# Kernel optimization log

Measured on AMD Instinct MI355X. Metric: run time of the kernel, lower is better.

Reference implementation:

```python
import jax, jax.numpy as jnp
import numpy as np

N, IN_DIM, OUT_DIM = 100000, 256, 256
EPS = 1e-6

def setup_inputs() -> dict:
    key = jax.random.key(0)
    ks = jax.random.split(key, 7)
    s = 1.0 / np.sqrt(IN_DIM)
    x = jax.random.normal(ks[0], (N, IN_DIM), dtype=jnp.float32)
    Wq = jax.random.uniform(ks[1], (IN_DIM, OUT_DIM), jnp.float32, -s, s)
    bq = jax.random.uniform(ks[2], (OUT_DIM,), jnp.float32, -s, s)
    Wk = jax.random.uniform(ks[3], (IN_DIM, OUT_DIM), jnp.float32, -s, s)
    bk = jax.random.uniform(ks[4], (OUT_DIM,), jnp.float32, -s, s)
    Wv = jax.random.uniform(ks[5], (IN_DIM, OUT_DIM), jnp.float32, -s, s)
    bv = jax.random.uniform(ks[6], (OUT_DIM,), jnp.float32, -s, s)
    return {"x": x, "Wq": Wq, "bq": bq, "Wk": Wk, "bk": bk, "Wv": Wv, "bv": bv}

def reference(x, Wq, bq, Wk, bk, Wv, bv):
    Q = jax.nn.relu(x @ Wq + bq)          # [N, d]
    K = jax.nn.relu(x @ Wk + bk)          # [N, d]
    V = x @ Wv + bv                       # [N, d]
    KV = jnp.einsum('nd,ne->de', K, V)    # [d, d]
    out = Q @ KV                          # [N, d]
    normalizer = Q @ K.sum(axis=0)[:, None].reshape(-1) [..., None] if False else (Q @ K.sum(axis=0)[:, None]) + EPS  # [N, 1]
    return out / normalizer
```

## Files before the change

### kernel.cpp

```cpp
#include <hip/hip_runtime.h>

typedef unsigned short u16;
typedef float f32x4 __attribute__((ext_vector_type(4)));
typedef short s16x8 __attribute__((ext_vector_type(8)));
typedef unsigned short u16x4 __attribute__((ext_vector_type(4)));

#define EPS 1e-6f

static __device__ __forceinline__ u16 f2bf(float f) {
  unsigned u = __float_as_uint(f);
  u += 0x7fffu + ((u >> 16) & 1u);
  return (u16)(u >> 16);
}
static __device__ __forceinline__ float bf2f(u16 h) {
  return __uint_as_float(((unsigned)h) << 16);
}

__global__ void wtrans_kernel(const float* __restrict__ Wq, const float* __restrict__ Wk,
                              const float* __restrict__ Wv,
                              u16* __restrict__ WqT, u16* __restrict__ WkT, u16* __restrict__ WvT) {
  int b = blockIdx.x;
  int mat = b >> 4, cg = b & 15;
  const float* W = mat == 0 ? Wq : (mat == 1 ? Wk : Wv);
  u16* WT = mat == 0 ? WqT : (mat == 1 ? WkT : WvT);
  int t = threadIdx.x;
  int c = cg * 16 + (t & 15);
  int k0 = (t >> 4) * 16;
  for (int i = 0; i < 16; ++i) {
    int k = k0 + i;
    WT[c * 256 + k] = f2bf(W[k * 256 + c]);
  }
}

__global__ __launch_bounds__(256, 2)
void qkv_kernel(const float* __restrict__ x,
                const u16* __restrict__ WqT, const u16* __restrict__ WkT, const u16* __restrict__ WvT,
                const float* __restrict__ bq, const float* __restrict__ bk, const float* __restrict__ bv,
                u16* __restrict__ Qb, u16* __restrict__ Kt, u16* __restrict__ Vt,
                float* __restrict__ ksum, int N, int NPAD) {
  __shared__ u16 xs[128][264];
  __shared__ u16 wst[128][40];
  __shared__ float ksl[256];
  const int tid = threadIdx.x;
  const int n0 = blockIdx.x * 128;

  ksl[tid] = 0.f;

  for (int i = 0; i < 32; ++i) {
    int l = tid + i * 256;
    int row = l >> 6;
    int c4 = (l & 63) << 2;
    int n = n0 + row;
    float4 v = make_float4(0.f, 0.f, 0.f, 0.f);
    if (n < N) v = *(const float4*)(x + (size_t)n * 256 + c4);
    u16x4 pk;
    pk[0] = f2bf(v.x); pk[1] = f2bf(v.y); pk[2] = f2bf(v.z); pk[3] = f2bf(v.w);
    *(u16x4*)&xs[row][c4] = pk;
  }

  const int wave = tid >> 6, lane = tid & 63;
  const int quad = lane >> 4, l16 = lane & 15;
  const int wr = (wave >> 1) * 64;
  const int wc = (wave & 1) * 64;

  const int scol = tid >> 1, sseg = (tid & 1) * 16;

  s16x8 w0, w1;
  {
    const u16* p = WqT + (size_t)scol * 256 + sseg;
    w0 = *(const s16x8*)p;
    w1 = *(const s16x8*)(p + 8);
  }

  f32x4 acc[4][4] = {};
  for (int it = 0; it < 48; ++it) {
    const int ph = it >> 3, kc = (it & 7) * 32;
    const int mat = ph >> 1;
    const int colBase = (ph & 1) * 128;

    __syncthreads();
    *(s16x8*)&wst[scol][sseg] = w0;
    *(s16x8*)&wst[scol][sseg + 8] = w1;
    __syncthreads();

    if (it + 1 < 48) {
      int itn = it + 1;
      int phn = itn >> 3, kcn = (itn & 7) * 32;
      int matn = phn >> 1, colBn = (phn & 1) * 128;
      const u16* WTn = matn == 0 ? WqT : (matn == 1 ? WkT : WvT);
      const u16* p = WTn + (size_t)(colBn + scol) * 256 + kcn + sseg;
      w0 = *(const s16x8*)p;
      w1 = *(const s16x8*)(p + 8);
    }

    s16x8 a[4], b[4];
    for (int f = 0; f < 4; ++f) a[f] = *(const s16x8*)&xs[wr + f * 16 + l16][kc + quad * 8];
    for (int f = 0; f < 4; ++f) b[f] = *(const s16x8*)&wst[wc + f * 16 + l16][quad * 8];
    for (int fr = 0; fr < 4; ++fr)
      for (int fc = 0; fc < 4; ++fc)
        acc[fr][fc] = __builtin_amdgcn_mfma_f32_16x16x32_bf16(a[fr], b[fc], acc[fr][fc], 0, 0, 0);

    if ((it & 7) == 7) {
      const float* bias = mat == 0 ? bq : (mat == 1 ? bk : bv);
      float ksacc[4] = {0.f, 0.f, 0.f, 0.f};
      for (int fc = 0; fc < 4; ++fc) {
        int colg = colBase + wc + fc * 16 + l16;
        float bb = bias[colg];
        for (int fr = 0; fr < 4; ++fr) {
          int nl = wr + fr * 16 + quad * 4;
          int n = n0 + nl;
          if (mat == 0) {
            for (int j = 0; j < 4; ++j) {
              float v = acc[fr][fc][j] + bb;
              v = fmaxf(v, 0.f);
              Qb[(size_t)(n + j) * 256 + colg] = (n + j < N) ? f2bf(v) : (u16)0;
            }
          } else {
            u16x4 pk;
            for (int j = 0; j < 4; ++j) {
              float v = acc[fr][fc][j] + bb;
              if (mat == 1) v = fmaxf(v, 0.f);
              bool ok = (n + j < N);
              pk[j] = ok ? f2bf(v) : (u16)0;
              if (mat == 1) ksacc[fc] += ok ? v : 0.f;
            }
            u16* T = (mat == 1) ? Kt : Vt;
            *(u16x4*)&T[(size_t)colg * NPAD + n] = pk;
          }
        }
      }
      if (mat == 1) {
        for (int fc = 0; fc < 4; ++fc) {
          float v = ksacc[fc];
          v += __shfl_xor(v, 16);
          v += __shfl_xor(v, 32);
          if (quad == 0) atomicAdd(&ksl[colBase + wc + fc * 16 + l16], v);
        }
      }
      for (int fr = 0; fr < 4; ++fr)
        for (int fc = 0; fc < 4; ++fc)
          acc[fr][fc] = (f32x4){0.f, 0.f, 0.f, 0.f};
    }
  }
  __syncthreads();
  atomicAdd(&ksum[tid], ksl[tid]);
}

__global__ __launch_bounds__(256, 2)
void kv_kernel(const u16* __restrict__ Kt, const u16* __restrict__ Vt,
               float* __restrict__ P, int NPAD) {
  __shared__ u16 As[128][40];
  __shared__ u16 Bs[128][40];
  const int tid = threadIdx.x;
  const int s = blockIdx.x & 63;
  const int tile = blockIdx.x >> 6;
  const int ti = (tile >> 1) * 128;
  const int tj = (tile & 1) * 128;
  const int wave = tid >> 6, lane = tid & 63;
  const int quad = lane >> 4, l16 = lane & 15;
  const int we = (wave >> 1) * 64;
  const int wd = (wave & 1) * 64;
  f32x4 acc[4][4] = {};
  const int NCH = NPAD >> 5;

  int row0 = (tid * 2) >> 2, seg0 = ((tid * 2) & 3) * 8;
  int row1 = (tid * 2 + 1) >> 2, seg1 = ((tid * 2 + 1) & 3) * 8;

  s16x8 ra0, ra1, rb0, rb1;
  int c = s;
  if (c < NCH) {
    int nb = c << 5;
    ra0 = *(const s16x8*)&Vt[(size_t)(ti + row0) * NPAD + nb + seg0];
    ra1 = *(const s16x8*)&Vt[(size_t)(ti + row1) * NPAD + nb + seg1];
    rb0 = *(const s16x8*)&Kt[(size_t)(tj + row0) * NPAD + nb + seg0];
    rb1 = *(const s16x8*)&Kt[(size_t)(tj + row1) * NPAD + nb + seg1];
  }
  for (; c < NCH; c += 64) {
    __syncthreads();
    *(s16x8*)&As[row0][seg0] = ra0;
    *(s16x8*)&As[row1][seg1] = ra1;
    *(s16x8*)&Bs[row0][seg0] = rb0;
    *(s16x8*)&Bs[row1][seg1] = rb1;
    __syncthreads();
    int cn = c + 64;
    if (cn < NCH) {
      int nb = cn << 5;
      ra0 = *(const s16x8*)&Vt[(size_t)(ti + row0) * NPAD + nb + seg0];
      ra1 = *(const s16x8*)&Vt[(size_t)(ti + row1) * NPAD + nb + seg1];
      rb0 = *(const s16x8*)&Kt[(size_t)(tj + row0) * NPAD + nb + seg0];
      rb1 = *(const s16x8*)&Kt[(size_t)(tj + row1) * NPAD + nb + seg1];
    }
    s16x8 a[4], b[4];
    for (int f = 0; f < 4; ++f) a[f] = *(const s16x8*)&As[we + f * 16 + l16][quad * 8];
    for (int f = 0; f < 4; ++f) b[f] = *(const s16x8*)&Bs[wd + f * 16 + l16][quad * 8];
    for (int fr = 0; fr < 4; ++fr)
      for (int fc = 0; fc < 4; ++fc)
        acc[fr][fc] = __builtin_amdgcn_mfma_f32_16x16x32_bf16(a[fr], b[fc], acc[fr][fc], 0, 0, 0);
  }
  float* Pp = P + (size_t)s * 65536;
  for (int fr = 0; fr < 4; ++fr)
    for (int fc = 0; fc < 4; ++fc) {
      int d = tj + wd + fc * 16 + l16;
      int e0 = ti + we + fr * 16 + quad * 4;
      *(f32x4*)&Pp[(size_t)d * 256 + e0] = acc[fr][fc];
    }
}

__global__ void kvred_kernel(const float* __restrict__ P, u16* __restrict__ KVtb) {
  int d = blockIdx.x;
  int e = threadIdx.x;
  float s = 0.f;
  for (int sp = 0; sp < 64; ++sp) s += P[(size_t)sp * 65536 + d * 256 + e];
  KVtb[e * 256 + d] = f2bf(s);
}

__global__ __launch_bounds__(256, 2)
void out_kernel(const u16* __restrict__ Qb, const u16* __restrict__ KVtb,
                const float* __restrict__ ksum, float* __restrict__ out,
                int N, int NPAD) {
  __shared__ u16 Qs[128][264];
  __shared__ u16 KVs[128][40];
  __shared__ float nrm[128];
  __shared__ float ks[256];
  __shared__ float nrmp[256];
  const int tid = threadIdx.x;
  const int r0 = blockIdx.x * 128;

  for (int i = 0; i < 16; ++i) {
    int l = tid + i * 256;
    int row = l >> 5;
    int seg = (l & 31) << 3;
    *(s16x8*)&Qs[row][seg] = *(const s16x8*)&Qb[(size_t)(r0 + row) * 256 + seg];
  }
  ks[tid] = ksum[tid];
  __syncthreads();

  {
    int r = tid & 127, h = tid >> 7;
    float sa = 0.f;
    for (int d = h * 128; d < h * 128 + 128; d += 8) {
      s16x8 q = *(const s16x8*)&Qs[r][d];
      for (int j = 0; j < 8; ++j) sa += bf2f((u16)q[j]) * ks[d + j];
    }
    nrmp[tid] = sa;
  }
  __syncthreads();
  if (tid < 128) nrm[tid] = nrmp[tid] + nrmp[tid + 128] + EPS;

  const int wave = tid >> 6, lane = tid & 63;
  const int quad = lane >> 4, l16 = lane & 15;
  const int we = (wave >> 1) * 64;
  const int wrw = (wave & 1) * 64;
  const int scol = tid >> 1, sseg = (tid & 1) * 16;

  s16x8 w0, w1;
  {
    const u16* p = KVtb + (size_t)scol * 256 + sseg;
    w0 = *(const s16x8*)p;
    w1 = *(const s16x8*)(p + 8);
  }

  f32x4 acc[4][4] = {};
  for (int it = 0; it < 16; ++it) {
    const int eh = it >> 3, kc = (it & 7) * 32;

    __syncthreads();
    *(s16x8*)&KVs[scol][sseg] = w0;
    *(s16x8*)&KVs[scol][sseg + 8] = w1;
    __syncthreads();

    if (it + 1 < 16) {
      int itn = it + 1;
      int ehn = itn >> 3, kcn = (itn & 7) * 32;
      const u16* p = KVtb + (size_t)(ehn * 128 + scol) * 256 + kcn + sseg;
      w0 = *(const s16x8*)p;
      w1 = *(const s16x8*)(p + 8);
    }

    s16x8 a[4], b[4];
    for (int f = 0; f < 4; ++f) a[f] = *(const s16x8*)&KVs[we + f * 16 + l16][quad * 8];
    for (int f = 0; f < 4; ++f) b[f] = *(const s16x8*)&Qs[wrw + f * 16 + l16][kc + quad * 8];
    for (int fr = 0; fr < 4; ++fr)
      for (int fc = 0; fc < 4; ++fc)
        acc[fr][fc] = __builtin_amdgcn_mfma_f32_16x16x32_bf16(a[fr], b[fc], acc[fr][fc], 0, 0, 0);

    if ((it & 7) == 7) {
      for (int fc = 0; fc < 4; ++fc) {
        int rl = wrw + fc * 16 + l16;
        int rg = r0 + rl;
        float inv = 1.0f / nrm[rl];
        if (rg < N) {
          for (int fr = 0; fr < 4; ++fr) {
            int eg = eh * 128 + we + fr * 16 + quad * 4;
            f32x4 o;
            o[0] = acc[fr][fc][0] * inv;
            o[1] = acc[fr][fc][1] * inv;
            o[2] = acc[fr][fc][2] * inv;
            o[3] = acc[fr][fc][3] * inv;
            *(f32x4*)&out[(size_t)rg * 256 + eg] = o;
          }
        }
      }
      for (int fr = 0; fr < 4; ++fr)
        for (int fc = 0; fc < 4; ++fc)
          acc[fr][fc] = (f32x4){0.f, 0.f, 0.f, 0.f};
    }
  }
}

extern "C" void kernel_launch(void* const* d_in, const int* in_sizes, int n_in,
                              void* d_out, int out_size, void* d_ws, size_t ws_size,
                              hipStream_t stream) {
  const float* x  = (const float*)d_in[0];
  const float* Wq = (const float*)d_in[1];
  const float* bq = (const float*)d_in[2];
  const float* Wk = (const float*)d_in[3];
  const float* bk = (const float*)d_in[4];
  const float* Wv = (const float*)d_in[5];
  const float* bv = (const float*)d_in[6];
  float* out = (float*)d_out;

  int N = in_sizes[0] / 256;
  int NPAD = ((N + 127) / 128) * 128;
  int nblk = NPAD / 128;

  char* p = (char*)d_ws;
  size_t szT = (size_t)256 * NPAD * sizeof(u16);
  u16* Kt = (u16*)p; p += szT;
  u16* Vt = (u16*)p; p += szT;
  u16* Qb = (u16*)p; p += szT;
  float* P = (float*)p; p += (size_t)64 * 65536 * sizeof(float);
  u16* KVtb = (u16*)p; p += (size_t)65536 * sizeof(u16);
  float* ksum = (float*)p; p += 256 * sizeof(float);
  u16* WqT = (u16*)p; p += (size_t)65536 * sizeof(u16);
  u16* WkT = (u16*)p; p += (size_t)65536 * sizeof(u16);
  u16* WvT = (u16*)p; p += (size_t)65536 * sizeof(u16);

  hipMemsetAsync(ksum, 0, 256 * sizeof(float), stream);
  wtrans_kernel<<<48, 256, 0, stream>>>(Wq, Wk, Wv, WqT, WkT, WvT);
  qkv_kernel<<<nblk, 256, 0, stream>>>(x, WqT, WkT, WvT, bq, bk, bv, Qb, Kt, Vt, ksum, N, NPAD);
  kv_kernel<<<256, 256, 0, stream>>>(Kt, Vt, P, NPAD);
  kvred_kernel<<<256, 256, 0, stream>>>(P, KVtb);
  out_kernel<<<nblk, 256, 0, stream>>>(Qb, KVtb, ksum, out, N, NPAD);
}
```

Before: 377.5 us.

## Double-buffer QKV and KV GEMM stages, enlarge QKV tiles, widen KV split

The QKV projection kernel now processes 256 rows per block with 512 threads and double-buffers the weight tile in shared memory, so each k-step needs one barrier instead of two. The Q epilogue uses swapped MFMA operands so Q can be stored as packed 4-element rows. The KV reduction kernel gets double-buffered shared tiles and a split factor of 128 when workspace allows, which doubles its grid. The trade-offs are higher LDS use per block, fewer QKV blocks in flight, and more partial sums for the reduce kernel to read.

Result: slower. 413.7 us (+9.6%).

```diff
diff --git a/kernel.cpp b/kernel.cpp
--- a/kernel.cpp
+++ b/kernel.cpp
@@ -32,22 +32,22 @@
   }
 }
 
-__global__ __launch_bounds__(256, 2)
+__global__ __launch_bounds__(512, 2)
 void qkv_kernel(const float* __restrict__ x,
                 const u16* __restrict__ WqT, const u16* __restrict__ WkT, const u16* __restrict__ WvT,
                 const float* __restrict__ bq, const float* __restrict__ bk, const float* __restrict__ bv,
                 u16* __restrict__ Qb, u16* __restrict__ Kt, u16* __restrict__ Vt,
                 float* __restrict__ ksum, int N, int NPAD) {
-  __shared__ u16 xs[128][264];
-  __shared__ u16 wst[128][40];
+  __shared__ u16 xs[256][264];
+  __shared__ u16 wst[2][128][40];
   __shared__ float ksl[256];
   const int tid = threadIdx.x;
-  const int n0 = blockIdx.x * 128;
-
-  ksl[tid] = 0.f;
+  const int n0 = blockIdx.x * 256;
+
+  if (tid < 256) ksl[tid] = 0.f;
 
   for (int i = 0; i < 32; ++i) {
-    int l = tid + i * 256;
+    int l = tid + i * 512;
     int row = l >> 6;
     int c4 = (l & 63) << 2;
     int n = n0 + row;
@@ -63,97 +63,125 @@
   const int wr = (wave >> 1) * 64;
   const int wc = (wave & 1) * 64;
 
-  const int scol = tid >> 1, sseg = (tid & 1) * 16;
-
-  s16x8 w0, w1;
-  {
-    const u16* p = WqT + (size_t)scol * 256 + sseg;
-    w0 = *(const s16x8*)p;
-    w1 = *(const s16x8*)(p + 8);
-  }
+  const int scol = tid >> 2, sseg = (tid & 3) * 8;
+
+  auto cptr = [&](int it) -> const u16* {
+    int ph = it >> 3, kc = (it & 7) * 32;
+    int mat = ph >> 1, colB = (ph & 1) * 128;
+    const u16* WT = mat == 0 ? WqT : (mat == 1 ? WkT : WvT);
+    return WT + (size_t)(colB + scol) * 256 + kc + sseg;
+  };
+
+#define QKV_MFMA(BUF, SWAP) { \
+    s16x8 a[4], b[4]; \
+    _Pragma("unroll") for (int f = 0; f < 4; ++f) a[f] = *(const s16x8*)&xs[wr + f * 16 + l16][kc + quad * 8]; \
+    _Pragma("unroll") for (int f = 0; f < 4; ++f) b[f] = *(const s16x8*)&wst[BUF][wc + f * 16 + l16][quad * 8]; \
+    if (SWAP) { \
+      _Pragma("unroll") for (int fr = 0; fr < 4; ++fr) \
+      _Pragma("unroll") for (int fc = 0; fc < 4; ++fc) \
+        acc[fr][fc] = __builtin_amdgcn_mfma_f32_16x16x32_bf16(b[fr], a[fc], acc[fr][fc], 0, 0, 0); \
+    } else { \
+      _Pragma("unroll") for (int fr = 0; fr < 4; ++fr) \
+      _Pragma("unroll") for (int fc = 0; fc < 4; ++fc) \
+        acc[fr][fc] = __builtin_amdgcn_mfma_f32_16x16x32_bf16(a[fr], b[fc], acc[fr][fc], 0, 0, 0); \
+    } }
+
+  s16x8 w0 = *(const s16x8*)cptr(0);
+  s16x8 w1 = *(const s16x8*)cptr(1);
+  *(s16x8*)&wst[0][scol][sseg] = w0;
 
   f32x4 acc[4][4] = {};
-  for (int it = 0; it < 48; ++it) {
-    const int ph = it >> 3, kc = (it & 7) * 32;
-    const int mat = ph >> 1;
-    const int colBase = (ph & 1) * 128;
-
-    __syncthreads();
-    *(s16x8*)&wst[scol][sseg] = w0;
-    *(s16x8*)&wst[scol][sseg + 8] = w1;
-    __syncthreads();
-
-    if (it + 1 < 48) {
-      int itn = it + 1;
-      int phn = itn >> 3, kcn = (itn & 7) * 32;
-      int matn = phn >> 1, colBn = (phn & 1) * 128;
-      const u16* WTn = matn == 0 ? WqT : (matn == 1 ? WkT : WvT);
-      const u16* p = WTn + (size_t)(colBn + scol) * 256 + kcn + sseg;
-      w0 = *(const s16x8*)p;
-      w1 = *(const s16x8*)(p + 8);
-    }
-
-    s16x8 a[4], b[4];
-    for (int f = 0; f < 4; ++f) a[f] = *(const s16x8*)&xs[wr + f * 16 + l16][kc + quad * 8];
-    for (int f = 0; f < 4; ++f) b[f] = *(const s16x8*)&wst[wc + f * 16 + l16][quad * 8];
-    for (int fr = 0; fr < 4; ++fr)
-      for (int fc = 0; fc < 4; ++fc)
-        acc[fr][fc] = __builtin_amdgcn_mfma_f32_16x16x32_bf16(a[fr], b[fc], acc[fr][fc], 0, 0, 0);
-
-    if ((it & 7) == 7) {
-      const float* bias = mat == 0 ? bq : (mat == 1 ? bk : bv);
-      float ksacc[4] = {0.f, 0.f, 0.f, 0.f};
-      for (int fc = 0; fc < 4; ++fc) {
-        int colg = colBase + wc + fc * 16 + l16;
-        float bb = bias[colg];
-        for (int fr = 0; fr < 4; ++fr) {
-          int nl = wr + fr * 16 + quad * 4;
-          int n = n0 + nl;
-          if (mat == 0) {
-            for (int j = 0; j < 4; ++j) {
-              float v = acc[fr][fc][j] + bb;
-              v = fmaxf(v, 0.f);
-              Qb[(size_t)(n + j) * 256 + colg] = (n + j < N) ? f2bf(v) : (u16)0;
+  for (int ii = 0; ii < 24; ++ii) {
+    {
+      const int it = 2 * ii;
+      const int kc = (it & 7) * 32;
+      const bool swapQ = (it < 16);
+      __syncthreads();
+      if (it < 46) w0 = *(const s16x8*)cptr(it + 2);
+      QKV_MFMA(0, swapQ);
+      *(s16x8*)&wst[1][scol][sseg] = w1;
+    }
+    {
+      const int it = 2 * ii + 1;
+      const int kc = (it & 7) * 32;
+      const int ph = it >> 3;
+      const int mat = ph >> 1, colBase = (ph & 1) * 128;
+      __syncthreads();
+      if (it < 46) w1 = *(const s16x8*)cptr(it + 2);
+      QKV_MFMA(1, (mat == 0));
+      if (it < 47) *(s16x8*)&wst[0][scol][sseg] = w0;
+
+      if ((it & 7) == 7) {
+        const float* bias = mat == 0 ? bq : (mat == 1 ? bk : bv);
+        if (mat == 0) {
+#pragma unroll
+          for (int fw = 0; fw < 4; ++fw) {
+            int colg4 = colBase + wc + fw * 16 + quad * 4;
+            float4 bb = *(const float4*)(bias + colg4);
+#pragma unroll
+            for (int fx = 0; fx < 4; ++fx) {
+              int n = n0 + wr + fx * 16 + l16;
+              u16x4 pk;
+              pk[0] = f2bf(fmaxf(acc[fw][fx][0] + bb.x, 0.f));
+              pk[1] = f2bf(fmaxf(acc[fw][fx][1] + bb.y, 0.f));
+              pk[2] = f2bf(fmaxf(acc[fw][fx][2] + bb.z, 0.f));
+              pk[3] = f2bf(fmaxf(acc[fw][fx][3] + bb.w, 0.f));
+              if (n >= N) { pk[0] = 0; pk[1] = 0; pk[2] = 0; pk[3] = 0; }
+              *(u16x4*)&Qb[(size_t)n * 256 + colg4] = pk;
             }
-          } else {
-            u16x4 pk;
-            for (int j = 0; j < 4; ++j) {
-              float v = acc[fr][fc][j] + bb;
-              if (mat == 1) v = fmaxf(v, 0.f);
-              bool ok = (n + j < N);
-              pk[j] = ok ? f2bf(v) : (u16)0;
-              if (mat == 1) ksacc[fc] += ok ? v : 0.f;
+          }
+        } else {
+          float ksacc[4] = {0.f, 0.f, 0.f, 0.f};
+#pragma unroll
+          for (int fc = 0; fc < 4; ++fc) {
+            int colg = colBase + wc + fc * 16 + l16;
+            float bb = bias[colg];
+#pragma unroll
+            for (int fr = 0; fr < 4; ++fr) {
+              int n = n0 + wr + fr * 16 + quad * 4;
+              u16x4 pk;
+#pragma unroll
+              for (int j = 0; j < 4; ++j) {
+                float v = acc[fr][fc][j] + bb;
+                if (mat == 1) v = fmaxf(v, 0.f);
+                bool ok = (n + j < N);
+                pk[j] = ok ? f2bf(v) : (u16)0;
+                if (mat == 1) ksacc[fc] += ok ? v : 0.f;
+              }
+              u16* T = (mat == 1) ? Kt : Vt;
+              *(u16x4*)&T[(size_t)colg * NPAD + n] = pk;
             }
-            u16* T = (mat == 1) ? Kt : Vt;
-            *(u16x4*)&T[(size_t)colg * NPAD + n] = pk;
+          }
+          if (mat == 1) {
+#pragma unroll
+            for (int fc = 0; fc < 4; ++fc) {
+              float v = ksacc[fc];
+              v += __shfl_xor(v, 16);
+              v += __shfl_xor(v, 32);
+              if (quad == 0) atomicAdd(&ksl[colBase + wc + fc * 16 + l16], v);
+            }
           }
         }
+#pragma unroll
+        for (int fr = 0; fr < 4; ++fr)
+#pragma unroll
+          for (int fc = 0; fc < 4; ++fc)
+            acc[fr][fc] = (f32x4){0.f, 0.f, 0.f, 0.f};
       }
-      if (mat == 1) {
-        for (int fc = 0; fc < 4; ++fc) {
-          float v = ksacc[fc];
-          v += __shfl_xor(v, 16);
-          v += __shfl_xor(v, 32);
-          if (quad == 0) atomicAdd(&ksl[colBase + wc + fc * 16 + l16], v);
-        }
-      }
-      for (int fr = 0; fr < 4; ++fr)
-        for (int fc = 0; fc < 4; ++fc)
-          acc[fr][fc] = (f32x4){0.f, 0.f, 0.f, 0.f};
     }
   }
   __syncthreads();
-  atomicAdd(&ksum[tid], ksl[tid]);
+  if (tid < 256) atomicAdd(&ksum[tid], ksl[tid]);
 }
 
 __global__ __launch_bounds__(256, 2)
 void kv_kernel(const u16* __restrict__ Kt, const u16* __restrict__ Vt,
-               float* __restrict__ P, int NPAD) {
-  __shared__ u16 As[128][40];
-  __shared__ u16 Bs[128][40];
+               float* __restrict__ P, int NPAD, int kvsplit, int kvlog) {
+  __shared__ u16 As[2][128][40];
+  __shared__ u16 Bs[2][128][40];
   const int tid = threadIdx.x;
-  const int s = blockIdx.x & 63;
-  const int tile = blockIdx.x >> 6;
+  const int s = blockIdx.x & (kvsplit - 1);
+  const int tile = blockIdx.x >> kvlog;
   const int ti = (tile >> 1) * 128;
   const int tj = (tile & 1) * 128;
   const int wave = tid >> 6, lane = tid & 63;
@@ -163,42 +191,53 @@
   f32x4 acc[4][4] = {};
   const int NCH = NPAD >> 5;
 
-  int row0 = (tid * 2) >> 2, seg0 = ((tid * 2) & 3) * 8;
-  int row1 = (tid * 2 + 1) >> 2, seg1 = ((tid * 2 + 1) & 3) * 8;
-
-  s16x8 ra0, ra1, rb0, rb1;
-  int c = s;
-  if (c < NCH) {
-    int nb = c << 5;
-    ra0 = *(const s16x8*)&Vt[(size_t)(ti + row0) * NPAD + nb + seg0];
-    ra1 = *(const s16x8*)&Vt[(size_t)(ti + row1) * NPAD + nb + seg1];
-    rb0 = *(const s16x8*)&Kt[(size_t)(tj + row0) * NPAD + nb + seg0];
-    rb1 = *(const s16x8*)&Kt[(size_t)(tj + row1) * NPAD + nb + seg1];
-  }
-  for (; c < NCH; c += 64) {
-    __syncthreads();
-    *(s16x8*)&As[row0][seg0] = ra0;
-    *(s16x8*)&As[row1][seg1] = ra1;
-    *(s16x8*)&Bs[row0][seg0] = rb0;
-    *(s16x8*)&Bs[row1][seg1] = rb1;
-    __syncthreads();
-    int cn = c + 64;
-    if (cn < NCH) {
-      int nb = cn << 5;
-      ra0 = *(const s16x8*)&Vt[(size_t)(ti + row0) * NPAD + nb + seg0];
-      ra1 = *(const s16x8*)&Vt[(size_t)(ti + row1) * NPAD + nb + seg1];
-      rb0 = *(const s16x8*)&Kt[(size_t)(tj + row0) * NPAD + nb + seg0];
-      rb1 = *(const s16x8*)&Kt[(size_t)(tj + row1) * NPAD + nb + seg1];
-    }
-    s16x8 a[4], b[4];
-    for (int f = 0; f < 4; ++f) a[f] = *(const s16x8*)&As[we + f * 16 + l16][quad * 8];
-    for (int f = 0; f < 4; ++f) b[f] = *(const s16x8*)&Bs[wd + f * 16 + l16][quad * 8];
-    for (int fr = 0; fr < 4; ++fr)
-      for (int fc = 0; fc < 4; ++fc)
-        acc[fr][fc] = __builtin_amdgcn_mfma_f32_16x16x32_bf16(a[fr], b[fc], acc[fr][fc], 0, 0, 0);
-  }
+  const int row0 = (tid * 2) >> 2, seg0 = ((tid * 2) & 3) * 8;
+  const int row1 = (tid * 2 + 1) >> 2, seg1 = ((tid * 2 + 1) & 3) * 8;
+
+  const int nit = (NCH - s + kvsplit - 1) / kvsplit;
+
+#define KV_LOAD(C, RA0, RA1, RB0, RB1) { int nb = (C) << 5; \
+    RA0 = *(const s16x8*)&Vt[(size_t)(ti + row0) * NPAD + nb + seg0]; \
+    RA1 = *(const s16x8*)&Vt[(size_t)(ti + row1) * NPAD + nb + seg1]; \
+    RB0 = *(const s16x8*)&Kt[(size_t)(tj + row0) * NPAD + nb + seg0]; \
+    RB1 = *(const s16x8*)&Kt[(size_t)(tj + row1) * NPAD + nb + seg1]; }
+
+#define KV_STORE(BUF, RA0, RA1, RB0, RB1) { \
+    *(s16x8*)&As[BUF][row0][seg0] = RA0; *(s16x8*)&As[BUF][row1][seg1] = RA1; \
+    *(s16x8*)&Bs[BUF][row0][seg0] = RB0; *(s16x8*)&Bs[BUF][row1][seg1] = RB1; }
+
+#define KV_MFMA(BUF) { s16x8 a[4], b[4]; \
+    _Pragma("unroll") for (int f = 0; f < 4; ++f) a[f] = *(const s16x8*)&As[BUF][we + f * 16 + l16][quad * 8]; \
+    _Pragma("unroll") for (int f = 0; f < 4; ++f) b[f] = *(const s16x8*)&Bs[BUF][wd + f * 16 + l16][quad * 8]; \
+    _Pragma("unroll") for (int fr = 0; fr < 4; ++fr) \
+    _Pragma("unroll") for (int fc = 0; fc < 4; ++fc) \
+      acc[fr][fc] = __builtin_amdgcn_mfma_f32_16x16x32_bf16(a[fr], b[fc], acc[fr][fc], 0, 0, 0); }
+
+  s16x8 xa0, xa1, xb0, xb1, ya0, ya1, yb0, yb1;
+  KV_LOAD(s, xa0, xa1, xb0, xb1);
+  if (nit > 1) KV_LOAD(s + kvsplit, ya0, ya1, yb0, yb1);
+  KV_STORE(0, xa0, xa1, xb0, xb1);
+
+  int t = 0;
+  for (; t + 1 < nit; t += 2) {
+    __syncthreads();
+    if (t + 2 < nit) KV_LOAD(s + (t + 2) * kvsplit, xa0, xa1, xb0, xb1);
+    KV_MFMA(0);
+    KV_STORE(1, ya0, ya1, yb0, yb1);
+    __syncthreads();
+    if (t + 3 < nit) KV_LOAD(s + (t + 3) * kvsplit, ya0, ya1, yb0, yb1);
+    KV_MFMA(1);
+    if (t + 2 < nit) KV_STORE(0, xa0, xa1, xb0, xb1);
+  }
+  if (t < nit) {
+    __syncthreads();
+    KV_MFMA(0);
+  }
+
   float* Pp = P + (size_t)s * 65536;
+#pragma unroll
   for (int fr = 0; fr < 4; ++fr)
+#pragma unroll
     for (int fc = 0; fc < 4; ++fc) {
       int d = tj + wd + fc * 16 + l16;
       int e0 = ti + we + fr * 16 + quad * 4;
@@ -206,11 +245,11 @@
     }
 }
 
-__global__ void kvred_kernel(const float* __restrict__ P, u16* __restrict__ KVtb) {
+__global__ void kvred_kernel(const float* __restrict__ P, u16* __restrict__ KVtb, int nsp) {
   int d = blockIdx.x;
   int e = threadIdx.x;
   float s = 0.f;
-  for (int sp = 0; sp < 64; ++sp) s += P[(size_t)sp * 65536 + d * 256 + e];
+  for (int sp = 0; sp < nsp; ++sp) s += P[(size_t)sp * 65536 + d * 256 + e];
   KVtb[e * 256 + d] = f2bf(s);
 }
 
@@ -240,6 +279,7 @@
     float sa = 0.f;
     for (int d = h * 128; d < h * 128 + 128; d += 8) {
       s16x8 q = *(const s16x8*)&Qs[r][d];
+#pragma unroll
       for (int j = 0; j < 8; ++j) sa += bf2f((u16)q[j]) * ks[d + j];
     }
     nrmp[tid] = sa;
@@ -278,18 +318,24 @@
     }
 
     s16x8 a[4], b[4];
+#pragma unroll
     for (int f = 0; f < 4; ++f) a[f] = *(const s16x8*)&KVs[we + f * 16 + l16][quad * 8];
+#pragma unroll
     for (int f = 0; f < 4; ++f) b[f] = *(const s16x8*)&Qs[wrw + f * 16 + l16][kc + quad * 8];
+#pragma unroll
     for (int fr = 0; fr < 4; ++fr)
+#pragma unroll
       for (int fc = 0; fc < 4; ++fc)
         acc[fr][fc] = __builtin_amdgcn_mfma_f32_16x16x32_bf16(a[fr], b[fc], acc[fr][fc], 0, 0, 0);
 
     if ((it & 7) == 7) {
+#pragma unroll
       for (int fc = 0; fc < 4; ++fc) {
         int rl = wrw + fc * 16 + l16;
         int rg = r0 + rl;
         float inv = 1.0f / nrm[rl];
         if (rg < N) {
+#pragma unroll
           for (int fr = 0; fr < 4; ++fr) {
             int eg = eh * 128 + we + fr * 16 + quad * 4;
             f32x4 o;
@@ -301,7 +347,9 @@
           }
         }
       }
+#pragma unroll
       for (int fr = 0; fr < 4; ++fr)
+#pragma unroll
         for (int fc = 0; fc < 4; ++fc)
           acc[fr][fc] = (f32x4){0.f, 0.f, 0.f, 0.f};
     }
@@ -321,15 +369,21 @@
   float* out = (float*)d_out;
 
   int N = in_sizes[0] / 256;
-  int NPAD = ((N + 127) / 128) * 128;
-  int nblk = NPAD / 128;
+  int NPAD = ((N + 255) / 256) * 256;
+  int nblkQ = NPAD / 256;
+  int nblkO = NPAD / 128;
+
+  size_t szT = (size_t)256 * NPAD * sizeof(u16);
+  size_t fixed = 3 * szT + (size_t)65536 * sizeof(u16) + 256 * sizeof(float)
+               + 3 * (size_t)65536 * sizeof(u16);
+  int kvsplit = 128, kvlog = 7;
+  if (fixed + (size_t)128 * 65536 * sizeof(float) > ws_size) { kvsplit = 64; kvlog = 6; }
 
   char* p = (char*)d_ws;
-  size_t szT = (size_t)256 * NPAD * sizeof(u16);
   u16* Kt = (u16*)p; p += szT;
   u16* Vt = (u16*)p; p += szT;
   u16* Qb = (u16*)p; p += szT;
-  float* P = (float*)p; p += (size_t)64 * 65536 * sizeof(float);
+  float* P = (float*)p; p += (size_t)kvsplit * 65536 * sizeof(float);
   u16* KVtb = (u16*)p; p += (size_t)65536 * sizeof(u16);
   float* ksum = (float*)p; p += 256 * sizeof(float);
   u16* WqT = (u16*)p; p += (size_t)65536 * sizeof(u16);
@@ -338,8 +392,8 @@
 
   hipMemsetAsync(ksum, 0, 256 * sizeof(float), stream);
   wtrans_kernel<<<48, 256, 0, stream>>>(Wq, Wk, Wv, WqT, WkT, WvT);
-  qkv_kernel<<<nblk, 256, 0, stream>>>(x, WqT, WkT, WvT, bq, bk, bv, Qb, Kt, Vt, ksum, N, NPAD);
-  kv_kernel<<<256, 256, 0, stream>>>(Kt, Vt, P, NPAD);
-  kvred_kernel<<<256, 256, 0, stream>>>(P, KVtb);
-  out_kernel<<<nblk, 256, 0, stream>>>(Qb, KVtb, ksum, out, N, NPAD);
-}
+  qkv_kernel<<<nblkQ, 512, 0, stream>>>(x, WqT, WkT, WvT, bq, bk, bv, Qb, Kt, Vt, ksum, N, NPAD);
+  kv_kernel<<<kvsplit * 4, 256, 0, stream>>>(Kt, Vt, P, NPAD, kvsplit, kvlog);
+  kvred_kernel<<<256, 256, 0, stream>>>(P, KVtb, kvsplit);
+  out_kernel<<<nblkO, 256, 0, stream>>>(Qb, KVtb, ksum, out, N, NPAD);
+}
```
